# Performance work log

Measured on AMD Instinct MI355X. Metric: run time of the kernel, lower is better.

Reference implementation:

```python
import jax, jax.numpy as jnp
import numpy as np
from jax import lax

EPS = 1e-12  # tf.nn.l2_normalize epsilon


def setup_inputs() -> dict:
    key = jax.random.key(0)
    k1, k2, k3 = jax.random.split(key, 3)
    B, T, D, C, F, K = 64, 2048, 1024, 1024, 256, 5
    sentence_embed = jax.random.normal(k1, (B, T, D), dtype=jnp.float32)
    label_embed = jax.random.normal(k2, (C, D), dtype=jnp.float32)
    conv_w = jax.random.normal(k3, (K, C, F), dtype=jnp.float32) * 0.05
    conv_b = jnp.zeros((F,), dtype=jnp.float32)
    return {"sentence_embed": sentence_embed, "label_embed": label_embed,
            "conv_w": conv_w, "conv_b": conv_b}


def reference(sentence_embed, label_embed, conv_w, conv_b):
    # l2-normalize label embeddings along feature dim (tf.nn.l2_normalize semantics)
    sq = jnp.sum(label_embed * label_embed, axis=-1, keepdims=True)
    label_norm = label_embed * lax.rsqrt(jnp.maximum(sq, EPS))
    # G: [B, T, C] = sentence_embed @ label_norm^T (raw sentence_embed, per original)
    G = jnp.einsum('btd,cd->btc', sentence_embed, label_norm)
    # Conv1D over time, 'same' padding, relu: [B, T, F]
    conv = lax.conv_general_dilated(
        G, conv_w, window_strides=(1,), padding='SAME',
        dimension_numbers=('NWC', 'WIO', 'NWC'))
    conv = jax.nn.relu(conv + conv_b)
    # max over filters -> attention values [B, T] (NOT softmaxed in original output path)
    att_v = jnp.max(conv, axis=-1)
    # batch_dot(sentence_embed, att_v, axes=[1,1]) -> [B, D]
    H_enc = jnp.einsum('btd,bt->bd', sentence_embed, att_v)
    return H_enc
```

## Files before the change

### kernel.cpp

```cpp
#include <hip/hip_runtime.h>

typedef unsigned short u16;
typedef __attribute__((ext_vector_type(4))) float f32x4;
typedef __attribute__((ext_vector_type(8))) short s16x8;
typedef __attribute__((ext_vector_type(4))) unsigned short u16x4;

#define DEV __device__ __forceinline__
#define VMW(N) asm volatile("s_waitcnt vmcnt(" #N ")" ::: "memory")
#define BARM() asm volatile("s_barrier" ::: "memory")
#define SCHEDB() __builtin_amdgcn_sched_barrier(0)

constexpr int Bb = 64, Tt = 2048, Dd = 1024, Cc = 1024, Ff = 256;
constexpr int TP = Tt + 4;
constexpr int M1 = Bb * Tt;

DEV u16 f2bf(float f) {
    union { float f; unsigned u; } v; v.f = f;
    unsigned r = v.u + 0x7fffu + ((v.u >> 16) & 1u);
    return (u16)(r >> 16);
}
DEV float bf2f(u16 h) {
    union { unsigned u; float f; } v; v.u = ((unsigned)h) << 16; return v.f;
}

DEV void gl_lds16(const u16* g, u16* l) {
    __builtin_amdgcn_global_load_lds(
        (const __attribute__((address_space(1))) unsigned*)(const void*)g,
        (__attribute__((address_space(3))) unsigned*)(void*)l,
        16, 0, 0);
}

DEV int swz_scol(int lane) { return (((lane & 7) ^ ((lane >> 3) & 7)) << 3); }
DEV int swz_rd(int row, int e) { return e ^ ((row & 7) << 3); }

__global__ __launch_bounds__(256) void k_s2bf(const float* __restrict__ S,
                                              u16* __restrict__ Sb) {
    size_t i = ((size_t)blockIdx.x * 256 + threadIdx.x) * 8;
    const size_t stride = (size_t)gridDim.x * 256 * 8;
    const size_t n = (size_t)M1 * Dd;
    for (; i < n; i += stride) {
        f32x4 a = *(const f32x4*)(S + i);
        f32x4 b = *(const f32x4*)(S + i + 4);
        s16x8 r;
        r[0] = (short)f2bf(a.x); r[1] = (short)f2bf(a.y);
        r[2] = (short)f2bf(a.z); r[3] = (short)f2bf(a.w);
        r[4] = (short)f2bf(b.x); r[5] = (short)f2bf(b.y);
        r[6] = (short)f2bf(b.z); r[7] = (short)f2bf(b.w);
        *(s16x8*)(Sb + i) = r;
    }
}

__global__ __launch_bounds__(256) void k_label_norm(const float* __restrict__ L,
                                                    u16* __restrict__ Ln) {
    int c = blockIdx.x;
    int t = threadIdx.x;
    const float* row = L + (size_t)c * Dd;
    float s = 0.f;
    for (int d = t; d < Dd; d += 256) { float v = row[d]; s += v * v; }
    for (int o = 32; o; o >>= 1) s += __shfl_down(s, o);
    __shared__ float red[4];
    if ((t & 63) == 0) red[t >> 6] = s;
    __syncthreads();
    float tot = red[0] + red[1] + red[2] + red[3];
    float r = rsqrtf(fmaxf(tot, 1e-12f));
    for (int d = t; d < Dd; d += 256) Ln[(size_t)c * Dd + d] = f2bf(row[d] * r);
}

__global__ __launch_bounds__(256) void k_wt(const float* __restrict__ W,
                                            u16* __restrict__ Wt) {
    __shared__ float tile[64][65];
    int k = blockIdx.x; int c0 = blockIdx.y * 64; int f0 = blockIdx.z * 64;
    int tid = threadIdx.x;
    const float* Wk = W + (size_t)k * Cc * Ff;
    #pragma unroll
    for (int i = 0; i < 16; ++i) {
        int q = tid + i * 256;
        int ci = q >> 6, fj = q & 63;
        tile[ci][fj] = Wk[(size_t)(c0 + ci) * Ff + f0 + fj];
    }
    __syncthreads();
    #pragma unroll
    for (int i = 0; i < 16; ++i) {
        int q = tid + i * 256;
        int fi = q >> 6, cj = q & 63;
        Wt[((size_t)k * Ff + f0 + fi) * Cc + c0 + cj] = f2bf(tile[cj][fi]);
    }
}

__global__ __launch_bounds__(256) void k_zpad(u16* __restrict__ Gp) {
    int b_ = blockIdx.x, tid = threadIdx.x;
    size_t base = (size_t)b_ * TP * Cc;
    for (int i = tid; i < 2 * Cc; i += 256) {
        Gp[base + i] = 0;
        Gp[base + (size_t)(TP - 2) * Cc + i] = 0;
    }
}

__global__ __launch_bounds__(512) void k_gemm1_8ph(const u16* __restrict__ Sb,
                                                   const u16* __restrict__ Ln,
                                                   u16* __restrict__ Gp) {
    __shared__ alignas(16) u16 As[2][256 * 64];
    __shared__ alignas(16) u16 Bs[2][256 * 64];
    int bid = blockIdx.x;
    int xcd = bid & 7, idx = bid >> 3;
    int mt = xcd * 64 + (idx >> 2);
    int nt = idx & 3;
    const int m0 = mt * 256, n0 = nt * 256;
    int tid = threadIdx.x, lane = tid & 63, wid = tid >> 6;
    int wm = wid >> 2, wn = wid & 3;
    int srow = lane >> 3, scol = swz_scol(lane);
    const int rsel = lane & 15;
    const int klo = (lane >> 4) * 8, khi = 32 + klo;
    f32x4 acc[8][4] = {};

    auto stageBfull = [&](int kt, int buf) {
        #pragma unroll
        for (int i = 0; i < 4; ++i) {
            int seg = wid * 4 + i;
            gl_lds16(Ln + (size_t)(n0 + seg * 8 + srow) * Dd + kt * 64 + scol,
                     &Bs[buf][seg * 512]);
        }
    };
    auto stageAh = [&](int kt, int h, int buf) {
        #pragma unroll
        for (int i = 0; i < 2; ++i) {
            int seg = h * 16 + wid * 2 + i;
            gl_lds16(Sb + (size_t)(m0 + seg * 8 + srow) * Dd + kt * 64 + scol,
                     &As[buf][seg * 512]);
        }
    };

    stageBfull(0, 0); stageAh(0, 0, 0);
    stageAh(0, 1, 0);
    VMW(2); SCHEDB(); BARM();

    for (int kt = 0; kt < 16; ++kt) {
        const int cur = kt & 1, nxt = cur ^ 1;
        const u16* Ab = As[cur];
        const u16* Bq = Bs[cur];
        s16x8 a[4], b[4];
        #pragma unroll
        for (int f = 0; f < 4; ++f) {
            int row = wm * 64 + f * 16 + rsel;
            a[f] = *(const s16x8*)&Ab[row * 64 + swz_rd(row, klo)];
        }
        #pragma unroll
        for (int f = 0; f < 4; ++f) {
            int row = wn * 64 + f * 16 + rsel;
            b[f] = *(const s16x8*)&Bq[row * 64 + swz_rd(row, klo)];
        }
        if (kt < 15) { stageBfull(kt + 1, nxt); stageAh(kt + 1, 0, nxt); }
        BARM();
        __builtin_amdgcn_s_setprio(1);
        #pragma unroll
        for (int fm = 0; fm < 4; ++fm)
            #pragma unroll
            for (int fn = 0; fn < 4; ++fn)
                acc[fm][fn] = __builtin_amdgcn_mfma_f32_16x16x32_bf16(
                    a[fm], b[fn], acc[fm][fn], 0, 0, 0);
        __builtin_amdgcn_s_setprio(0);
        if (kt < 15) { VMW(6); } else { VMW(0); }
        SCHEDB();
        BARM();
        #pragma unroll
        for (int f = 0; f < 4; ++f) {
            int row = 128 + wm * 64 + f * 16 + rsel;
            a[f] = *(const s16x8*)&Ab[row * 64 + swz_rd(row, klo)];
        }
        if (kt < 15) stageAh(kt + 1, 1, nxt);
        BARM();
        __builtin_amdgcn_s_setprio(1);
        #pragma unroll
        for (int fm = 0; fm < 4; ++fm)
            #pragma unroll
            for (int fn = 0; fn < 4; ++fn)
                acc[4 + fm][fn] = __builtin_amdgcn_mfma_f32_16x16x32_bf16(
                    a[fm], b[fn], acc[4 + fm][fn], 0, 0, 0);
        __builtin_amdgcn_s_setprio(0);
        BARM();
        #pragma unroll
        for (int f = 0; f < 4; ++f) {
            int row = wm * 64 + f * 16 + rsel;
            a[f] = *(const s16x8*)&Ab[row * 64 + swz_rd(row, khi)];
        }
        #pragma unroll
        for (int f = 0; f < 4; ++f) {
            int row = wn * 64 + f * 16 + rsel;
            b[f] = *(const s16x8*)&Bq[row * 64 + swz_rd(row, khi)];
        }
        BARM();
        __builtin_amdgcn_s_setprio(1);
        #pragma unroll
        for (int fm = 0; fm < 4; ++fm)
            #pragma unroll
            for (int fn = 0; fn < 4; ++fn)
                acc[fm][fn] = __builtin_amdgcn_mfma_f32_16x16x32_bf16(
                    a[fm], b[fn], acc[fm][fn], 0, 0, 0);
        __builtin_amdgcn_s_setprio(0);
        BARM();
        #pragma unroll
        for (int f = 0; f < 4; ++f) {
            int row = 128 + wm * 64 + f * 16 + rsel;
            a[f] = *(const s16x8*)&Ab[row * 64 + swz_rd(row, khi)];
        }
        BARM();
        __builtin_amdgcn_s_setprio(1);
        #pragma unroll
        for (int fm = 0; fm < 4; ++fm)
            #pragma unroll
            for (int fn = 0; fn < 4; ++fn)
                acc[4 + fm][fn] = __builtin_amdgcn_mfma_f32_16x16x32_bf16(
                    a[fm], b[fn], acc[4 + fm][fn], 0, 0, 0);
        __builtin_amdgcn_s_setprio(0);
        VMW(2); SCHEDB(); BARM();
    }
    #pragma unroll
    for (int m = 0; m < 8; ++m) {
        #pragma unroll
        for (int r = 0; r < 4; ++r) {
            int row = m0 + (m >> 2) * 128 + wm * 64 + (m & 3) * 16 + (lane >> 4) * 4 + r;
            int b_ = row >> 11, t = row & 2047;
            size_t base = ((size_t)b_ * TP + t + 2) * Cc;
            #pragma unroll
            for (int n = 0; n < 4; ++n) {
                int col = n0 + wn * 64 + n * 16 + rsel;
                Gp[base + col] = f2bf(acc[m][n][r]);
            }
        }
    }
}

__global__ __launch_bounds__(256) void k_gemm1_f32(const float* __restrict__ S,
                                                   const u16* __restrict__ Ln,
                                                   u16* __restrict__ Gp) {
    __shared__ alignas(16) u16 As[128 * 64];
    __shared__ alignas(16) u16 Bs[128 * 64];
    int bid = blockIdx.x;
    int xcd = bid & 7, idx = bid >> 3;
    int mt = xcd * 128 + (idx >> 3);
    int nt = idx & 7;
    const int m0 = mt * 128, n0 = nt * 128;
    int tid = threadIdx.x;
    int lane = tid & 63, wid = tid >> 6;
    int wm = wid >> 1, wn = wid & 1;
    f32x4 acc[4][4] = {};

    for (int kt = 0; kt < 16; ++kt) {
        int k0 = kt * 64;
        #pragma unroll
        for (int i = 0; i < 8; ++i) {
            int q = tid + i * 256;
            int row = q >> 4, c4 = (q & 15) * 4;
            f32x4 v = *(const f32x4*)(S + (size_t)(m0 + row) * Dd + k0 + c4);
            u16* p = &As[row * 64 + c4];
            p[0] = f2bf(v.x); p[1] = f2bf(v.y); p[2] = f2bf(v.z); p[3] = f2bf(v.w);
        }
        #pragma unroll
        for (int i = 0; i < 4; ++i) {
            int q = tid + i * 256;
            int row = q >> 3, c8 = (q & 7) * 8;
            *(s16x8*)&Bs[row * 64 + c8] =
                *(const s16x8*)(Ln + (size_t)(n0 + row) * Dd + k0 + c8);
        }
        __syncthreads();
        #pragma unroll
        for (int kk = 0; kk < 2; ++kk) {
            int rsel = lane & 15, ksel = kk * 32 + (lane >> 4) * 8;
            s16x8 a[4], b[4];
            #pragma unroll
            for (int f = 0; f < 4; ++f)
                a[f] = *(const s16x8*)&As[(wm * 64 + f * 16 + rsel) * 64 + ksel];
            #pragma unroll
            for (int f = 0; f < 4; ++f)
                b[f] = *(const s16x8*)&Bs[(wn * 64 + f * 16 + rsel) * 64 + ksel];
            #pragma unroll
            for (int fm = 0; fm < 4; ++fm)
                #pragma unroll
                for (int fn = 0; fn < 4; ++fn)
                    acc[fm][fn] = __builtin_amdgcn_mfma_f32_16x16x32_bf16(
                        a[fm], b[fn], acc[fm][fn], 0, 0, 0);
        }
        __syncthreads();
    }
    #pragma unroll
    for (int fm = 0; fm < 4; ++fm) {
        #pragma unroll
        for (int r = 0; r < 4; ++r) {
            int row = m0 + wm * 64 + fm * 16 + (lane >> 4) * 4 + r;
            int b_ = row >> 11, t = row & 2047;
            size_t base = ((size_t)b_ * TP + t + 2) * Cc;
            #pragma unroll
            for (int fn = 0; fn < 4; ++fn) {
                int col = n0 + wn * 64 + fn * 16 + (lane & 15);
                Gp[base + col] = f2bf(acc[fm][fn][r]);
            }
        }
    }
}

__global__ __launch_bounds__(512) void k_conv(const u16* __restrict__ Gp,
                                              const u16* __restrict__ Wt,
                                              const float* __restrict__ bias,
                                              float* __restrict__ att) {
    __shared__ alignas(16) u16 As[2][40 * 512];
    __shared__ alignas(16) u16 Bs[2][256 * 64];
    __shared__ float red[2][256];
    int mt = blockIdx.x;
    int b_ = mt >> 3;
    int t0 = (mt & 7) * 256;
    int tid = threadIdx.x, lane = tid & 63, wid = tid >> 6;
    int wm = wid >> 1, wn = wid & 1;
    int srow = lane >> 3, scol = swz_scol(lane);
    f32x4 acc[4][8] = {};
    const size_t gbase = ((size_t)b_ * TP + t0) * Cc;

    auto stage_B = [&](int s2) {
        int ct2 = s2 / 5, k2 = s2 % 5, buf = s2 & 1;
        #pragma unroll
        for (int i = 0; i < 4; ++i) {
            int seg = wid * 4 + i;
            gl_lds16(Wt + ((size_t)k2 * Ff + seg * 8 + srow) * Cc + ct2 * 64 + scol,
                     &Bs[buf][seg * 512]);
        }
    };
    auto stage_A = [&](int ct2) {
        int buf = ct2 & 1;
        #pragma unroll
        for (int i = 0; i < 5; ++i) {
            int seg = wid * 5 + i;
            gl_lds16(Gp + gbase + (size_t)(seg * 8 + srow) * Cc + ct2 * 64 + scol,
                     &As[buf][seg * 512]);
        }
    };
    auto compute = [&](int cb, int ca, int k) {
        #pragma unroll
        for (int kk = 0; kk < 2; ++kk) {
            int rsel = lane & 15, ksel = kk * 32 + (lane >> 4) * 8;
            s16x8 a[4], b[8];
            #pragma unroll
            for (int f = 0; f < 4; ++f) {
                int row = k + wm * 64 + f * 16 + rsel;
                a[f] = *(const s16x8*)&As[ca][row * 64 + swz_rd(row, ksel)];
            }
            #pragma unroll
            for (int f = 0; f < 8; ++f) {
                int row = wn * 128 + f * 16 + rsel;
                b[f] = *(const s16x8*)&Bs[cb][row * 64 + swz_rd(row, ksel)];
            }
            #pragma unroll
            for (int fm = 0; fm < 4; ++fm)
                #pragma unroll
                for (int fn = 0; fn < 8; ++fn)
                    acc[fm][fn] = __builtin_amdgcn_mfma_f32_16x16x32_bf16(
                        a[fm], b[fn], acc[fm][fn], 0, 0, 0);
        }
    };

    stage_A(0); stage_B(0); stage_B(1);

    for (int ct = 0; ct < 15; ++ct) {
        int s = ct * 5, ca = ct & 1;
        VMW(4); SCHEDB(); BARM();
        compute(s & 1, ca, 0);
        BARM();
        stage_B(s + 2); stage_A(ct + 1);
        VMW(9); SCHEDB(); BARM();
        compute((s + 1) & 1, ca, 1);
        BARM();
        stage_B(s + 3);
        VMW(9); SCHEDB(); BARM();
        compute((s + 2) & 1, ca, 2);
        BARM();
        stage_B(s + 4);
        VMW(4); SCHEDB(); BARM();
        compute((s + 3) & 1, ca, 3);
        BARM();
        stage_B(s + 5);
        VMW(4); SCHEDB(); BARM();
        compute((s + 4) & 1, ca, 4);
        BARM();
        stage_B(s + 6);
    }
    VMW(4); SCHEDB(); BARM(); compute(1, 1, 0); BARM(); stage_B(77);
    VMW(4); SCHEDB(); BARM(); compute(0, 1, 1); BARM(); stage_B(78);
    VMW(4); SCHEDB(); BARM(); compute(1, 1, 2); BARM(); stage_B(79);
    VMW(4); SCHEDB(); BARM(); compute(0, 1, 3); BARM();
    VMW(0); SCHEDB(); BARM(); compute(1, 1, 4); BARM();

    float bv[8];
    #pragma unroll
    for (int fn = 0; fn < 8; ++fn)
        bv[fn] = bias[wn * 128 + fn * 16 + (lane & 15)];
    #pragma unroll
    for (int fm = 0; fm < 4; ++fm) {
        #pragma unroll
        for (int r = 0; r < 4; ++r) {
            float v = 0.f;
            #pragma unroll
            for (int fn = 0; fn < 8; ++fn)
                v = fmaxf(v, fmaxf(acc[fm][fn][r] + bv[fn], 0.f));
            #pragma unroll
            for (int m = 1; m <= 8; m <<= 1) v = fmaxf(v, __shfl_xor(v, m));
            if ((lane & 15) == 0)
                red[wn][wm * 64 + fm * 16 + (lane >> 4) * 4 + r] = v;
        }
    }
    __syncthreads();
    if (tid < 256)
        att[(size_t)mt * 256 + tid] = fmaxf(red[0][tid], red[1][tid]);
}

__global__ __launch_bounds__(256) void k_henc_bf(const u16* __restrict__ Sb,
                                                 const float* __restrict__ att,
                                                 float* __restrict__ part) {
    int b_ = blockIdx.x, tc = blockIdx.y;
    int tid = threadIdx.x;
    int d = tid * 4;
    const u16* Sp = Sb + ((size_t)b_ * Tt + (size_t)tc * 256) * Dd + d;
    const float* ap = att + (size_t)b_ * Tt + (size_t)tc * 256;
    f32x4 acc = {};
    for (int t = 0; t < 256; ++t) {
        float a = ap[t];
        u16x4 s = *(const u16x4*)(Sp + (size_t)t * Dd);
        acc.x += bf2f(s.x) * a;
        acc.y += bf2f(s.y) * a;
        acc.z += bf2f(s.z) * a;
        acc.w += bf2f(s.w) * a;
    }
    *(f32x4*)(part + ((size_t)tc * Bb + b_) * Dd + d) = acc;
}

__global__ __launch_bounds__(256) void k_henc_f32(const float* __restrict__ S,
                                                  const float* __restrict__ att,
                                                  float* __restrict__ part) {
    int b_ = blockIdx.x, tc = blockIdx.y;
    int tid = threadIdx.x;
    int d = tid * 4;
    const float* Sp = S + ((size_t)b_ * Tt + (size_t)tc * 256) * Dd + d;
    const float* ap = att + (size_t)b_ * Tt + (size_t)tc * 256;
    f32x4 acc = {};
    for (int t = 0; t < 256; ++t) {
        float a = ap[t];
        f32x4 s = *(const f32x4*)(Sp + (size_t)t * Dd);
        acc += s * a;
    }
    *(f32x4*)(part + ((size_t)tc * Bb + b_) * Dd + d) = acc;
}

__global__ __launch_bounds__(256) void k_hred(const float* __restrict__ part,
                                              float* __restrict__ out) {
    int i = blockIdx.x * 256 + threadIdx.x;
    float s = 0.f;
    #pragma unroll
    for (int p = 0; p < 8; ++p) s += part[(size_t)p * (Bb * Dd) + i];
    out[i] = s;
}

extern "C" void kernel_launch(void* const* d_in, const int* in_sizes, int n_in,
                              void* d_out, int out_size, void* d_ws, size_t ws_size,
                              hipStream_t stream) {
    const float* S  = (const float*)d_in[0];
    const float* L  = (const float*)d_in[1];
    const float* W  = (const float*)d_in[2];
    const float* cb = (const float*)d_in[3];
    float* out = (float*)d_out;
    char* ws = (char*)d_ws;

    const size_t GP_B   = (size_t)Bb * TP * Cc * 2;
    const size_t LN_B   = (size_t)Cc * Dd * 2;
    const size_t WT_B   = (size_t)5 * Ff * Cc * 2;
    const size_t ATT_B  = (size_t)M1 * 4;
    const size_t PART_B = (size_t)8 * Bb * Dd * 4;
    const size_t SB_B   = (size_t)M1 * Dd * 2;
    u16*   Gp   = (u16*)(ws);
    u16*   Ln   = (u16*)(ws + GP_B);
    u16*   Wt   = (u16*)(ws + GP_B + LN_B);
    float* att  = (float*)(ws + GP_B + LN_B + WT_B);
    float* part = (float*)(ws + GP_B + LN_B + WT_B + ATT_B);
    u16*   Sb   = (u16*)(ws + GP_B + LN_B + WT_B + ATT_B + PART_B);
    const bool use_bf = ws_size >= GP_B + LN_B + WT_B + ATT_B + PART_B + SB_B;

    k_label_norm<<<Cc, 256, 0, stream>>>(L, Ln);
    k_wt<<<dim3(5, Cc / 64, Ff / 64), 256, 0, stream>>>(W, Wt);
    k_zpad<<<Bb, 256, 0, stream>>>(Gp);
    if (use_bf) {
        k_s2bf<<<2048, 256, 0, stream>>>(S, Sb);
        k_gemm1_8ph<<<(M1 / 256) * (Cc / 256), 512, 0, stream>>>(Sb, Ln, Gp);
    } else {
        k_gemm1_f32<<<(M1 / 128) * (Cc / 128), 256, 0, stream>>>(S, Ln, Gp);
    }
    k_conv<<<M1 / 256, 512, 0, stream>>>(Gp, Wt, cb, att);
    if (use_bf) k_henc_bf<<<dim3(Bb, 8), 256, 0, stream>>>(Sb, att, part);
    else        k_henc_f32<<<dim3(Bb, 8), 256, 0, stream>>>(S, att, part);
    k_hred<<<(Bb * Dd) / 256, 256, 0, stream>>>(part, out);
}
```

Before: 829.1 us.

## Simplify GEMM1 mainloop to prefetch-two-ahead double buffer with 128-row warp tiles

Replaces the 8-phase interleaved GEMM mainloop, which had many barriers and split A staging, with a simpler loop. Each iteration waits on the current buffer, computes the full 64-wide K slice, then issues loads for tile kt+2 into the freed buffer. The warp layout changes so each wave covers 128 rows by 64 columns, loading 8 A fragments per K step instead of recomputing halves. This removes many barriers and LDS re-reads. In exchange it holds more registers and loses the fine-grained interleave of loads and MFMAs.

After: 819.7 us. About the same (-1.1%).

```diff
diff --git a/kernel.cpp b/kernel.cpp
--- a/kernel.cpp
+++ b/kernel.cpp
@@ -96,9 +96,9 @@
     }
 }
 
-__global__ __launch_bounds__(512) void k_gemm1_8ph(const u16* __restrict__ Sb,
-                                                   const u16* __restrict__ Ln,
-                                                   u16* __restrict__ Gp) {
+__global__ __launch_bounds__(512) void k_gemm1_t4(const u16* __restrict__ Sb,
+                                                  const u16* __restrict__ Ln,
+                                                  u16* __restrict__ Gp) {
     __shared__ alignas(16) u16 As[2][256 * 64];
     __shared__ alignas(16) u16 Bs[2][256 * 64];
     int bid = blockIdx.x;
@@ -110,10 +110,17 @@
     int wm = wid >> 2, wn = wid & 3;
     int srow = lane >> 3, scol = swz_scol(lane);
     const int rsel = lane & 15;
-    const int klo = (lane >> 4) * 8, khi = 32 + klo;
     f32x4 acc[8][4] = {};
 
-    auto stageBfull = [&](int kt, int buf) {
+    auto stageA = [&](int kt, int buf) {
+        #pragma unroll
+        for (int i = 0; i < 4; ++i) {
+            int seg = wid * 4 + i;
+            gl_lds16(Sb + (size_t)(m0 + seg * 8 + srow) * Dd + kt * 64 + scol,
+                     &As[buf][seg * 512]);
+        }
+    };
+    auto stageB = [&](int kt, int buf) {
         #pragma unroll
         for (int i = 0; i < 4; ++i) {
             int seg = wid * 4 + i;
@@ -121,104 +128,48 @@
                      &Bs[buf][seg * 512]);
         }
     };
-    auto stageAh = [&](int kt, int h, int buf) {
-        #pragma unroll
-        for (int i = 0; i < 2; ++i) {
-            int seg = h * 16 + wid * 2 + i;
-            gl_lds16(Sb + (size_t)(m0 + seg * 8 + srow) * Dd + kt * 64 + scol,
-                     &As[buf][seg * 512]);
-        }
-    };
-
-    stageBfull(0, 0); stageAh(0, 0, 0);
-    stageAh(0, 1, 0);
-    VMW(2); SCHEDB(); BARM();
+    auto compute = [&](int buf) {
+        #pragma unroll
+        for (int kk = 0; kk < 2; ++kk) {
+            int ksel = kk * 32 + (lane >> 4) * 8;
+            s16x8 a[8], b[4];
+            #pragma unroll
+            for (int f = 0; f < 8; ++f) {
+                int row = wm * 128 + f * 16 + rsel;
+                a[f] = *(const s16x8*)&As[buf][row * 64 + swz_rd(row, ksel)];
+            }
+            #pragma unroll
+            for (int f = 0; f < 4; ++f) {
+                int row = wn * 64 + f * 16 + rsel;
+                b[f] = *(const s16x8*)&Bs[buf][row * 64 + swz_rd(row, ksel)];
+            }
+            __builtin_amdgcn_s_setprio(1);
+            #pragma unroll
+            for (int fm = 0; fm < 8; ++fm)
+                #pragma unroll
+                for (int fn = 0; fn < 4; ++fn)
+                    acc[fm][fn] = __builtin_amdgcn_mfma_f32_16x16x32_bf16(
+                        a[fm], b[fn], acc[fm][fn], 0, 0, 0);
+            __builtin_amdgcn_s_setprio(0);
+        }
+    };
+
+    stageA(0, 0); stageB(0, 0);
+    stageA(1, 1); stageB(1, 1);
 
     for (int kt = 0; kt < 16; ++kt) {
-        const int cur = kt & 1, nxt = cur ^ 1;
-        const u16* Ab = As[cur];
-        const u16* Bq = Bs[cur];
-        s16x8 a[4], b[4];
-        #pragma unroll
-        for (int f = 0; f < 4; ++f) {
-            int row = wm * 64 + f * 16 + rsel;
-            a[f] = *(const s16x8*)&Ab[row * 64 + swz_rd(row, klo)];
-        }
-        #pragma unroll
-        for (int f = 0; f < 4; ++f) {
-            int row = wn * 64 + f * 16 + rsel;
-            b[f] = *(const s16x8*)&Bq[row * 64 + swz_rd(row, klo)];
-        }
-        if (kt < 15) { stageBfull(kt + 1, nxt); stageAh(kt + 1, 0, nxt); }
-        BARM();
-        __builtin_amdgcn_s_setprio(1);
-        #pragma unroll
-        for (int fm = 0; fm < 4; ++fm)
-            #pragma unroll
-            for (int fn = 0; fn < 4; ++fn)
-                acc[fm][fn] = __builtin_amdgcn_mfma_f32_16x16x32_bf16(
-                    a[fm], b[fn], acc[fm][fn], 0, 0, 0);
-        __builtin_amdgcn_s_setprio(0);
-        if (kt < 15) { VMW(6); } else { VMW(0); }
-        SCHEDB();
-        BARM();
-        #pragma unroll
-        for (int f = 0; f < 4; ++f) {
-            int row = 128 + wm * 64 + f * 16 + rsel;
-            a[f] = *(const s16x8*)&Ab[row * 64 + swz_rd(row, klo)];
-        }
-        if (kt < 15) stageAh(kt + 1, 1, nxt);
-        BARM();
-        __builtin_amdgcn_s_setprio(1);
-        #pragma unroll
-        for (int fm = 0; fm < 4; ++fm)
-            #pragma unroll
-            for (int fn = 0; fn < 4; ++fn)
-                acc[4 + fm][fn] = __builtin_amdgcn_mfma_f32_16x16x32_bf16(
-                    a[fm], b[fn], acc[4 + fm][fn], 0, 0, 0);
-        __builtin_amdgcn_s_setprio(0);
-        BARM();
-        #pragma unroll
-        for (int f = 0; f < 4; ++f) {
-            int row = wm * 64 + f * 16 + rsel;
-            a[f] = *(const s16x8*)&Ab[row * 64 + swz_rd(row, khi)];
-        }
-        #pragma unroll
-        for (int f = 0; f < 4; ++f) {
-            int row = wn * 64 + f * 16 + rsel;
-            b[f] = *(const s16x8*)&Bq[row * 64 + swz_rd(row, khi)];
-        }
-        BARM();
-        __builtin_amdgcn_s_setprio(1);
-        #pragma unroll
-        for (int fm = 0; fm < 4; ++fm)
-            #pragma unroll
-            for (int fn = 0; fn < 4; ++fn)
-                acc[fm][fn] = __builtin_amdgcn_mfma_f32_16x16x32_bf16(
-                    a[fm], b[fn], acc[fm][fn], 0, 0, 0);
-        __builtin_amdgcn_s_setprio(0);
-        BARM();
-        #pragma unroll
-        for (int f = 0; f < 4; ++f) {
-            int row = 128 + wm * 64 + f * 16 + rsel;
-            a[f] = *(const s16x8*)&Ab[row * 64 + swz_rd(row, khi)];
-        }
-        BARM();
-        __builtin_amdgcn_s_setprio(1);
-        #pragma unroll
-        for (int fm = 0; fm < 4; ++fm)
-            #pragma unroll
-            for (int fn = 0; fn < 4; ++fn)
-                acc[4 + fm][fn] = __builtin_amdgcn_mfma_f32_16x16x32_bf16(
-                    a[fm], b[fn], acc[4 + fm][fn], 0, 0, 0);
-        __builtin_amdgcn_s_setprio(0);
-        VMW(2); SCHEDB(); BARM();
-    }
+        if (kt < 15) { VMW(8); } else { VMW(0); }
+        SCHEDB(); BARM();
+        compute(kt & 1);
+        BARM();
+        if (kt < 14) { stageA(kt + 2, kt & 1); stageB(kt + 2, kt & 1); }
+    }
+
     #pragma unroll
     for (int m = 0; m < 8; ++m) {
         #pragma unroll
         for (int r = 0; r < 4; ++r) {
-            int row = m0 + (m >> 2) * 128 + wm * 64 + (m & 3) * 16 + (lane >> 4) * 4 + r;
+            int row = m0 + wm * 128 + m * 16 + (lane >> 4) * 4 + r;
             int b_ = row >> 11, t = row & 2047;
             size_t base = ((size_t)b_ * TP + t + 2) * Cc;
             #pragma unroll
@@ -485,7 +436,7 @@
     k_zpad<<<Bb, 256, 0, stream>>>(Gp);
     if (use_bf) {
         k_s2bf<<<2048, 256, 0, stream>>>(S, Sb);
-        k_gemm1_8ph<<<(M1 / 256) * (Cc / 256), 512, 0, stream>>>(Sb, Ln, Gp);
+        k_gemm1_t4<<<(M1 / 256) * (Cc / 256), 512, 0, stream>>>(Sb, Ln, Gp);
     } else {
         k_gemm1_f32<<<(M1 / 128) * (Cc / 128), 256, 0, stream>>>(S, Ln, Gp);
     }
```
